# Performance work log

Hardware: AMD Instinct MI355X
Metric: run time of the kernel (lower is better)

The kernel has to match this reference:

```python
import jax, jax.numpy as jnp
import numpy as np

DIM = 128
DIM_HEAD = 32
HEADS = DIM // DIM_HEAD  # 4
WS = 25                  # window_size -> N = 625 tokens
SCALE = DIM_HEAD ** -0.5
BATCH = 256


def _rel_pos_indices(ws: int) -> np.ndarray:
    pos = np.arange(ws)
    grid = np.stack(np.meshgrid(pos, pos, indexing='ij')).reshape(2, -1).T  # (n, 2)
    rel = grid[:, None, :] - grid[None, :, :] + (ws - 1)                     # (n, n, 2)
    return rel[..., 0] * (2 * ws - 1) + rel[..., 1]                          # (n, n)


def setup_inputs() -> dict:
    key = jax.random.key(0)
    k1, k2, k3, k4 = jax.random.split(key, 4)
    x = jax.random.normal(k1, (BATCH, DIM, WS, WS), jnp.float32)
    W_qkv = jax.random.normal(k2, (3 * DIM, DIM), jnp.float32) * 0.02   # nn.Linear(dim, 3*dim, bias=False)
    W_out = jax.random.normal(k3, (DIM, DIM), jnp.float32) * 0.02       # nn.Linear(dim, dim, bias=False)
    bias_table = jax.random.normal(k4, ((2 * WS - 1) ** 2, HEADS), jnp.float32) * 0.02
    rel_pos_indices = jnp.asarray(_rel_pos_indices(WS), jnp.int32)      # (n, n)
    return {"x": x, "W_qkv": W_qkv, "W_out": W_out,
            "bias_table": bias_table, "rel_pos_indices": rel_pos_indices}


def reference(x, W_qkv, W_out, bias_table, rel_pos_indices):
    b, d, h, w = x.shape
    n = h * w
    xf = x.reshape(b, d, n).transpose(0, 2, 1)                 # b n d
    qkv = xf @ W_qkv.T                                          # b n 3d
    q, k, v = jnp.split(qkv, 3, axis=-1)
    split_heads = lambda t: t.reshape(b, n, HEADS, DIM_HEAD).transpose(0, 2, 1, 3)  # b h n dh
    q = split_heads(q) * SCALE
    k = split_heads(k)
    v = split_heads(v)
    sim = jnp.einsum('bhid,bhjd->bhij', q, k)                   # b h n n
    bias = bias_table[rel_pos_indices]                          # n n h
    sim = sim + bias.transpose(2, 0, 1)[None]                   # + h n n
    attn = jax.nn.softmax(sim, axis=-1)
    out = jnp.einsum('bhij,bhjd->bhid', attn, v)                # b h n dh
    out = out.transpose(0, 2, 1, 3).reshape(b, n, d)            # b n (h dh), head-major
    out = out @ W_out.T                                          # b n d
    return out.transpose(0, 2, 1).reshape(b, d, h, w)           # b d h w
```

## Files before the change

kernel.cpp:

```cpp
#include <hip/hip_runtime.h>
#include <hip/hip_bf16.h>


typedef __attribute__((ext_vector_type(8)))  short short8;
typedef __attribute__((ext_vector_type(4)))  float f32x4;
typedef __attribute__((ext_vector_type(16))) float f32x16;

#define MFMA16(a, b, c) __builtin_amdgcn_mfma_f32_16x16x32_bf16((a), (b), (c), 0, 0, 0)
#define MFMA32(a, b, c) __builtin_amdgcn_mfma_f32_32x32x16_bf16((a), (b), (c), 0, 0, 0)

__device__ __forceinline__ unsigned short f2b(float f) {
  __hip_bfloat16 h = __float2bfloat16(f);
  return *reinterpret_cast<unsigned short*>(&h);
}
__device__ __forceinline__ float b2f(unsigned short s) {
  union { unsigned u; float f; } x; x.u = ((unsigned)s) << 16;
  return x.f;
}
__device__ __forceinline__ unsigned cvtpk(float lo, float hi) {
  unsigned r;
  asm("v_cvt_pk_bf16_f32 %0, %1, %2" : "=v"(r) : "v"(lo), "v"(hi));
  return r;
}
__device__ __forceinline__ void pl32swap(unsigned& a, unsigned& b) {
  asm("v_permlane32_swap_b32 %0, %1" : "+v"(a), "+v"(b));
}

constexpr float LOG2E_F = 1.4426950408889634f;
constexpr float QSCALE  = 0.17677669529663687f * 1.4426950408889634f;

__global__ __launch_bounds__(256) void k_prep(const float* __restrict__ wqkv,
                                              const float* __restrict__ wout,
                                              unsigned short* __restrict__ wq_bf,
                                              unsigned short* __restrict__ wo_bf) {
  int id = blockIdx.x * 256 + threadIdx.x;
  if (id < 49152) wq_bf[id] = f2b(wqkv[id]);
  else            wo_bf[id - 49152] = f2b(wout[id - 49152]);
}

__global__ __launch_bounds__(256) void k_bias(const float* __restrict__ table,
                                              const int* __restrict__ idx,
                                              unsigned short* __restrict__ bt) {
  int id = blockIdx.x * 256 + threadIdx.x;
  int jg = id / 640, i = id % 640;
  float v[4][4];
#pragma unroll
  for (int e = 0; e < 4; ++e) {
    int j = jg * 4 + e;
    if (j >= 625) {
#pragma unroll
      for (int h = 0; h < 4; ++h) v[e][h] = -1e30f;
    } else if (i >= 625) {
#pragma unroll
      for (int h = 0; h < 4; ++h) v[e][h] = 0.f;
    } else {
      const float* tr = table + idx[i * 625 + j] * 4;
#pragma unroll
      for (int h = 0; h < 4; ++h) v[e][h] = tr[h] * LOG2E_F;
    }
  }
#pragma unroll
  for (int h = 0; h < 4; ++h) {
    ushort4 p;
    p.x = f2b(v[0][h]); p.y = f2b(v[1][h]); p.z = f2b(v[2][h]); p.w = f2b(v[3][h]);
    *reinterpret_cast<ushort4*>(bt + (size_t)h * 409600 + (size_t)id * 4) = p;
  }
}

__global__ __launch_bounds__(256) void k_qkv(const float* __restrict__ x,
                                             const unsigned short* __restrict__ wbf,
                                             unsigned short* __restrict__ qws,
                                             unsigned short* __restrict__ kws,
                                             unsigned short* __restrict__ vtws) {
  __shared__ float Xf[128 * 65];
  int blk = blockIdx.x;
  int b = blk / 10, tile = blk % 10;
  int t = threadIdx.x, w = t >> 6, lane = t & 63, r16 = lane & 15, g = lane >> 4;
  short8 wf[6][4];
#pragma unroll
  for (int f = 0; f < 6; ++f)
#pragma unroll
    for (int kk = 0; kk < 4; ++kk)
      wf[f][kk] = *reinterpret_cast<const short8*>(
          wbf + ((6 * w + f) * 16 + r16) * 128 + kk * 32 + g * 8);
  int n0 = tile * 64;
  const float* xb = x + (size_t)b * 80000;
  for (int it = 0; it < 32; ++it) {
    int idx = it * 256 + t;
    int d = idx >> 6, nc = idx & 63;
    int n = n0 + nc;
    Xf[d * 65 + nc] = (n < 625) ? xb[d * 625 + n] : 0.f;
  }
  __syncthreads();
  for (int rg = 0; rg < 4; ++rg) {
    int nr = n0 + rg * 16;
    short8 a[4];
#pragma unroll
    for (int kk = 0; kk < 4; ++kk) {
      short8 av;
#pragma unroll
      for (int jj = 0; jj < 8; ++jj)
        av[jj] = (short)f2b(Xf[(kk * 32 + g * 8 + jj) * 65 + rg * 16 + r16]);
      a[kk] = av;
    }
    f32x4 acc[6];
#pragma unroll
    for (int f = 0; f < 6; ++f) acc[f] = (f32x4){0.f, 0.f, 0.f, 0.f};
#pragma unroll
    for (int kk = 0; kk < 4; ++kk)
#pragma unroll
      for (int f = 0; f < 6; ++f)
        acc[f] = MFMA16(a[kk], wf[f][kk], acc[f]);
#pragma unroll
    for (int f = 0; f < 6; ++f) {
      int c0 = (6 * w + f) * 16;
      int sel = c0 >> 7, hh = (c0 & 127) >> 5, t0 = (c0 & 31);
      float mul = (sel == 0) ? QSCALE : 1.f;
      size_t base = (size_t)(b * 4 + hh);
      if (sel < 2) {
        unsigned short* dst = (sel ? kws : qws) + (base * 640 + nr + 4 * g) * 32 + t0 + r16;
#pragma unroll
        for (int rr = 0; rr < 4; ++rr) dst[rr * 32] = f2b(acc[f][rr] * mul);
      } else {
        ushort4 pv;
        pv.x = f2b(acc[f][0]); pv.y = f2b(acc[f][1]);
        pv.z = f2b(acc[f][2]); pv.w = f2b(acc[f][3]);
        *reinterpret_cast<ushort4*>(vtws + (base * 32 + t0 + r16) * 640 + nr + 4 * g) = pv;
      }
    }
  }
}

__global__ __launch_bounds__(512) void k_attn(const unsigned short* __restrict__ qws,
                                              const unsigned short* __restrict__ kws,
                                              const unsigned short* __restrict__ vtws,
                                              const unsigned short* __restrict__ bt,
                                              unsigned short* __restrict__ ows) {
  __shared__ __align__(16) unsigned short Kl[640 * 40];
  __shared__ __align__(16) unsigned short Vl[32 * 648];
  int bh = blockIdx.x, b = bh >> 2, h = bh & 3;
  int t = threadIdx.x, w = t >> 6, lane = t & 63;
  int i31 = lane & 31, hi = lane >> 5;
  const unsigned short* Kg = kws + (size_t)bh * 20480;
  const unsigned short* Vg = vtws + (size_t)bh * 20480;
  for (int it = 0; it < 5; ++it) {
    int idx = it * 512 + t;
    int row = idx >> 2, c8 = (idx & 3) * 8;
    *reinterpret_cast<short8*>(&Kl[row * 40 + c8]) =
        *reinterpret_cast<const short8*>(Kg + row * 32 + c8);
  }
  for (int it = 0; it < 5; ++it) {
    int idx = it * 512 + t;
    int d = idx / 80, nb = (idx % 80) * 8;
    *reinterpret_cast<short8*>(&Vl[d * 648 + nb]) =
        *reinterpret_cast<const short8*>(Vg + d * 640 + nb);
  }
  __syncthreads();
  const unsigned short* Qg = qws + (size_t)bh * 20480;
  const unsigned short* bth = bt + (size_t)h * 409600;
  short8 ones;
#pragma unroll
  for (int jj = 0; jj < 8; ++jj) ones[jj] = (short)0x3F80;

  for (int ti = w; ti < 20; ti += 8) {
    int i = ti * 32 + i31;
    short8 qf0 = *reinterpret_cast<const short8*>(Qg + i * 32 + hi * 8);
    short8 qf1 = *reinterpret_cast<const short8*>(Qg + i * 32 + 16 + hi * 8);
    f32x16 oacc, sacc;
#pragma unroll
    for (int r = 0; r < 16; ++r) { oacc[r] = 0.f; sacc[r] = 0.f; }
    for (int c = 0; c < 5; ++c) {
      int j0 = c * 128;
      f32x16 s[4];
#pragma unroll
      for (int jt = 0; jt < 4; ++jt) {
#pragma unroll
        for (int q = 0; q < 4; ++q) {
          int jg = (j0 >> 2) + jt * 8 + q * 2 + hi;
          ushort4 bv = *reinterpret_cast<const ushort4*>(bth + ((size_t)jg * 640 + i) * 4);
          s[jt][4 * q + 0] = b2f(bv.x);
          s[jt][4 * q + 1] = b2f(bv.y);
          s[jt][4 * q + 2] = b2f(bv.z);
          s[jt][4 * q + 3] = b2f(bv.w);
        }
      }
#pragma unroll
      for (int jt = 0; jt < 4; ++jt) {
        const unsigned short* kr = &Kl[(j0 + jt * 32 + i31) * 40 + hi * 8];
        short8 kf0 = *reinterpret_cast<const short8*>(kr);
        short8 kf1 = *reinterpret_cast<const short8*>(kr + 16);
        s[jt] = MFMA32(kf0, qf0, s[jt]);
        s[jt] = MFMA32(kf1, qf1, s[jt]);
      }
#pragma unroll
      for (int jt = 0; jt < 4; ++jt)
#pragma unroll
        for (int r = 0; r < 16; ++r) s[jt][r] = __builtin_amdgcn_exp2f(s[jt][r]);
      unsigned pk[4][4][2];
#pragma unroll
      for (int jt = 0; jt < 4; ++jt)
#pragma unroll
        for (int m = 0; m < 4; ++m) {
          pk[jt][m][0] = cvtpk(s[jt][4 * m + 0], s[jt][4 * m + 1]);
          pk[jt][m][1] = cvtpk(s[jt][4 * m + 2], s[jt][4 * m + 3]);
        }
#pragma unroll
      for (int ks = 0; ks < 8; ++ks) {
        int jt = ks >> 1, mb = 2 * (ks & 1);
        unsigned a0 = pk[jt][mb][0],     a1 = pk[jt][mb][1];
        unsigned b0 = pk[jt][mb + 1][0], b1 = pk[jt][mb + 1][1];
        pl32swap(a0, b0);
        pl32swap(a1, b1);
        uint4 fr = make_uint4(a0, a1, b0, b1);
        short8 pfrag = *reinterpret_cast<short8*>(&fr);
        short8 vf = *reinterpret_cast<const short8*>(&Vl[i31 * 648 + j0 + ks * 16 + hi * 8]);
        oacc = MFMA32(vf, pfrag, oacc);
        sacc = MFMA32(ones, pfrag, sacc);
      }
    }
    float rc = __builtin_amdgcn_rcpf(sacc[0]);
    size_t ob = ((size_t)b * 640 + i) * 128 + h * 32;
#pragma unroll
    for (int q = 0; q < 4; ++q)
#pragma unroll
      for (int h2 = 0; h2 < 2; ++h2) {
        unsigned pr = cvtpk(oacc[4 * q + 2 * h2] * rc, oacc[4 * q + 2 * h2 + 1] * rc);
        *reinterpret_cast<unsigned*>(ows + ob + q * 8 + hi * 4 + 2 * h2) = pr;
      }
  }
}

__global__ __launch_bounds__(256) void k_out(const unsigned short* __restrict__ ows,
                                             const unsigned short* __restrict__ wbf,
                                             float* __restrict__ out) {
  int blk = blockIdx.x;
  int b = blk / 10, tile = blk % 10;
  int t = threadIdx.x, w = t >> 6, lane = t & 63, r16 = lane & 15, g = lane >> 4;
  const unsigned short* Ob = ows + (size_t)b * 640 * 128;
  float* outb = out + (size_t)b * 128 * 625;
  int n0 = tile * 64;
  f32x4 acc[2][4];
#pragma unroll
  for (int mi = 0; mi < 2; ++mi)
#pragma unroll
    for (int f = 0; f < 4; ++f) acc[mi][f] = (f32x4){0.f, 0.f, 0.f, 0.f};
#pragma unroll
  for (int kk = 0; kk < 4; ++kk) {
    short8 bfr[4];
#pragma unroll
    for (int f = 0; f < 4; ++f)
      bfr[f] = *reinterpret_cast<const short8*>(Ob + (n0 + f * 16 + r16) * 128 + kk * 32 + g * 8);
#pragma unroll
    for (int mi = 0; mi < 2; ++mi) {
      short8 afr = *reinterpret_cast<const short8*>(wbf + (w * 32 + mi * 16 + r16) * 128 + kk * 32 + g * 8);
#pragma unroll
      for (int f = 0; f < 4; ++f) acc[mi][f] = MFMA16(afr, bfr[f], acc[mi][f]);
    }
  }
#pragma unroll
  for (int mi = 0; mi < 2; ++mi)
#pragma unroll
    for (int f = 0; f < 4; ++f) {
      int n = n0 + f * 16 + r16;
      if (n < 625) {
        int dout = w * 32 + mi * 16 + 4 * g;
        outb[(dout + 0) * 625 + n] = acc[mi][f][0];
        outb[(dout + 1) * 625 + n] = acc[mi][f][1];
        outb[(dout + 2) * 625 + n] = acc[mi][f][2];
        outb[(dout + 3) * 625 + n] = acc[mi][f][3];
      }
    }
}

extern "C" void kernel_launch(void* const* d_in, const int* in_sizes, int n_in,
                              void* d_out, int out_size, void* d_ws, size_t ws_size,
                              hipStream_t stream) {
  const float* x     = (const float*)d_in[0];
  const float* wqkv  = (const float*)d_in[1];
  const float* wout  = (const float*)d_in[2];
  const float* table = (const float*)d_in[3];
  const int*   idx   = (const int*)d_in[4];
  float* out = (float*)d_out;

  char* ws = (char*)d_ws;
  unsigned short* qws   = (unsigned short*)(ws);
  unsigned short* kws   = (unsigned short*)(ws + 41943040);
  unsigned short* vtws  = (unsigned short*)(ws + 83886080);
  unsigned short* ows   = (unsigned short*)(ws + 125829120);
  unsigned short* bt    = (unsigned short*)(ws + 167772160);
  unsigned short* wq_bf = (unsigned short*)(ws + 171048960);
  unsigned short* wo_bf = (unsigned short*)(ws + 171147264);

  k_prep<<<dim3(256), dim3(256), 0, stream>>>(wqkv, wout, wq_bf, wo_bf);
  k_bias<<<dim3(400), dim3(256), 0, stream>>>(table, idx, bt);
  k_qkv<<<dim3(2560), dim3(256), 0, stream>>>(x, wq_bf, qws, kws, vtws);
  k_attn<<<dim3(1024), dim3(512), 0, stream>>>(qws, kws, vtws, bt, ows);
  k_out<<<dim3(2560), dim3(256), 0, stream>>>(ows, wo_bf, out);
}
```

Baseline: 275.4 us.

## Split x transpose into separate bf16 kernel and halve QKV work per block

Adds a k_xpose kernel that converts x to bf16 and transposes it into a token-major workspace. k_qkv then reads MFMA A operands directly from global memory instead of staging fp32 through LDS, and each block now computes half the output columns, doubling the grid to 5120 blocks with fewer weight registers per wave. The aim is to shrink LDS use and register pressure and raise occupancy in the QKV projection. The cost is an extra kernel launch plus a write and re-read of the transposed x, and each x tile is now loaded by two blocks.

```diff
diff --git a/kernel.cpp b/kernel.cpp
--- a/kernel.cpp
+++ b/kernel.cpp
@@ -38,6 +38,30 @@
   else            wo_bf[id - 49152] = f2b(wout[id - 49152]);
 }
 
+__global__ __launch_bounds__(256) void k_xpose(const float* __restrict__ x,
+                                               unsigned short* __restrict__ xt) {
+  __shared__ unsigned short Xl[128 * 65];
+  int blk = blockIdx.x;
+  int b = blk / 10, tile = blk % 10;
+  int n0 = tile * 64, t = threadIdx.x;
+  const float* xb = x + (size_t)b * 80000;
+  for (int it = 0; it < 32; ++it) {
+    int idx = it * 256 + t;
+    int d = idx >> 6, nc = idx & 63, n = n0 + nc;
+    Xl[d * 65 + nc] = (n < 625) ? f2b(xb[d * 625 + n]) : (unsigned short)0;
+  }
+  __syncthreads();
+  unsigned short* xtb = xt + ((size_t)b * 640 + n0) * 128;
+  for (int it = 0; it < 4; ++it) {
+    int idx = it * 256 + t;
+    int row = idx >> 4, c8 = (idx & 15) * 8;
+    short8 v;
+#pragma unroll
+    for (int jj = 0; jj < 8; ++jj) v[jj] = (short)Xl[(c8 + jj) * 65 + row];
+    *reinterpret_cast<short8*>(xtb + row * 128 + c8) = v;
+  }
+}
+
 __global__ __launch_bounds__(256) void k_bias(const float* __restrict__ table,
                                               const int* __restrict__ idx,
                                               unsigned short* __restrict__ bt) {
@@ -67,53 +91,42 @@
   }
 }
 
-__global__ __launch_bounds__(256) void k_qkv(const float* __restrict__ x,
+__global__ __launch_bounds__(256) void k_qkv(const unsigned short* __restrict__ xt,
                                              const unsigned short* __restrict__ wbf,
                                              unsigned short* __restrict__ qws,
                                              unsigned short* __restrict__ kws,
                                              unsigned short* __restrict__ vtws) {
-  __shared__ float Xf[128 * 65];
   int blk = blockIdx.x;
-  int b = blk / 10, tile = blk % 10;
+  int cf = blk & 1, btl = blk >> 1;
+  int b = btl / 10, tile = btl % 10;
   int t = threadIdx.x, w = t >> 6, lane = t & 63, r16 = lane & 15, g = lane >> 4;
-  short8 wf[6][4];
-#pragma unroll
-  for (int f = 0; f < 6; ++f)
+  int F0 = cf * 12 + w * 3;
+  short8 wf[3][4];
+#pragma unroll
+  for (int f = 0; f < 3; ++f)
 #pragma unroll
     for (int kk = 0; kk < 4; ++kk)
       wf[f][kk] = *reinterpret_cast<const short8*>(
-          wbf + ((6 * w + f) * 16 + r16) * 128 + kk * 32 + g * 8);
-  int n0 = tile * 64;
-  const float* xb = x + (size_t)b * 80000;
-  for (int it = 0; it < 32; ++it) {
-    int idx = it * 256 + t;
-    int d = idx >> 6, nc = idx & 63;
-    int n = n0 + nc;
-    Xf[d * 65 + nc] = (n < 625) ? xb[d * 625 + n] : 0.f;
-  }
-  __syncthreads();
+          wbf + ((F0 + f) * 16 + r16) * 128 + kk * 32 + g * 8);
+  const unsigned short* xb = xt + ((size_t)b * 640 + tile * 64) * 128;
+#pragma unroll
   for (int rg = 0; rg < 4; ++rg) {
-    int nr = n0 + rg * 16;
     short8 a[4];
 #pragma unroll
-    for (int kk = 0; kk < 4; ++kk) {
-      short8 av;
-#pragma unroll
-      for (int jj = 0; jj < 8; ++jj)
-        av[jj] = (short)f2b(Xf[(kk * 32 + g * 8 + jj) * 65 + rg * 16 + r16]);
-      a[kk] = av;
-    }
-    f32x4 acc[6];
-#pragma unroll
-    for (int f = 0; f < 6; ++f) acc[f] = (f32x4){0.f, 0.f, 0.f, 0.f};
-#pragma unroll
     for (int kk = 0; kk < 4; ++kk)
-#pragma unroll
-      for (int f = 0; f < 6; ++f)
+      a[kk] = *reinterpret_cast<const short8*>(xb + (rg * 16 + r16) * 128 + kk * 32 + g * 8);
+    f32x4 acc[3];
+#pragma unroll
+    for (int f = 0; f < 3; ++f) acc[f] = (f32x4){0.f, 0.f, 0.f, 0.f};
+#pragma unroll
+    for (int kk = 0; kk < 4; ++kk)
+#pragma unroll
+      for (int f = 0; f < 3; ++f)
         acc[f] = MFMA16(a[kk], wf[f][kk], acc[f]);
-#pragma unroll
-    for (int f = 0; f < 6; ++f) {
-      int c0 = (6 * w + f) * 16;
+    int nr = tile * 64 + rg * 16;
+#pragma unroll
+    for (int f = 0; f < 3; ++f) {
+      int c0 = (F0 + f) * 16;
       int sel = c0 >> 7, hh = (c0 & 127) >> 5, t0 = (c0 & 31);
       float mul = (sel == 0) ? QSCALE : 1.f;
       size_t base = (size_t)(b * 4 + hh);
@@ -290,10 +303,12 @@
   unsigned short* bt    = (unsigned short*)(ws + 167772160);
   unsigned short* wq_bf = (unsigned short*)(ws + 171048960);
   unsigned short* wo_bf = (unsigned short*)(ws + 171147264);
+  unsigned short* xtws  = (unsigned short*)(ws + 171180032);
 
   k_prep<<<dim3(256), dim3(256), 0, stream>>>(wqkv, wout, wq_bf, wo_bf);
   k_bias<<<dim3(400), dim3(256), 0, stream>>>(table, idx, bt);
-  k_qkv<<<dim3(2560), dim3(256), 0, stream>>>(x, wq_bf, qws, kws, vtws);
+  k_xpose<<<dim3(2560), dim3(256), 0, stream>>>(x, xtws);
+  k_qkv<<<dim3(5120), dim3(256), 0, stream>>>(xtws, wq_bf, qws, kws, vtws);
   k_attn<<<dim3(1024), dim3(512), 0, stream>>>(qws, kws, vtws, bt, ows);
   k_out<<<dim3(2560), dim3(256), 0, stream>>>(ows, wo_bf, out);
 }
```

New measurement: 278.9 us. About the same (+1.3%).
